# Kernel tuning notes

Hardware: AMD Instinct MI355X
Metric: run time of the kernel (lower is better)

The kernel has to match this reference:

```python
import jax, jax.numpy as jnp
import numpy as np

DIM = 1024
DEPTH = 6
HEADS = 16
MLP = 4096
HEAD_DIM = DIM // HEADS
SCALE = HEAD_DIM ** -0.5
EPS = 1e-5


def _ln(x, g, b):
    m = jnp.mean(x, axis=-1, keepdims=True)
    v = jnp.mean(jnp.square(x - m), axis=-1, keepdims=True)
    return (x - m) * jax.lax.rsqrt(v + EPS) * g + b


def setup_inputs() -> dict:
    key = jax.random.key(0)
    ks = jax.random.split(key, 16)
    B, N = 4, 1024
    s_d = 1.0 / np.sqrt(DIM)
    s_m = 1.0 / np.sqrt(MLP)
    inp = {
        "x1": jax.random.normal(ks[0], (B, N, DIM), jnp.float32),
        "x2": jax.random.normal(ks[1], (B, N, DIM), jnp.float32),
        # stacked per-layer params; Linear weights stored as [in, out]
        "ln1_g": jnp.ones((DEPTH, DIM), jnp.float32),
        "ln1_b": jnp.zeros((DEPTH, DIM), jnp.float32),
        "wq": jax.random.normal(ks[2], (DEPTH, DIM, DIM), jnp.float32) * s_d,
        "wk": jax.random.normal(ks[3], (DEPTH, DIM, DIM), jnp.float32) * s_d,
        "wv": jax.random.normal(ks[4], (DEPTH, DIM, DIM), jnp.float32) * s_d,
        "wo": jax.random.normal(ks[5], (DEPTH, DIM, DIM), jnp.float32) * s_d,
        "bo": jnp.zeros((DEPTH, DIM), jnp.float32),
        "ln2_g": jnp.ones((DEPTH, DIM), jnp.float32),
        "ln2_b": jnp.zeros((DEPTH, DIM), jnp.float32),
        "w1": jax.random.normal(ks[6], (DEPTH, DIM, MLP), jnp.float32) * s_d,
        "b1": jnp.zeros((DEPTH, MLP), jnp.float32),
        "w2": jax.random.normal(ks[7], (DEPTH, MLP, DIM), jnp.float32) * s_m,
        "b2": jnp.zeros((DEPTH, DIM), jnp.float32),
    }
    return inp


def _split_heads(t):
    b, n, _ = t.shape
    return t.reshape(b, n, HEADS, HEAD_DIM).transpose(0, 2, 1, 3)  # b h n d


def reference(x1, x2, ln1_g, ln1_b, wq, wk, wv, wo, bo, ln2_g, ln2_b, w1, b1, w2, b2):
    # dropout disabled (eval mode)
    for i in range(DEPTH):
        # PreNorm(MCA): same LayerNorm params applied to x1 and x2
        n1 = _ln(x1, ln1_g[i], ln1_b[i])
        n2 = _ln(x2, ln1_g[i], ln1_b[i])
        q = _split_heads(n1 @ wq[i])
        k = _split_heads(n2 @ wk[i])
        v = _split_heads(n2 @ wv[i])
        dots = jnp.einsum('bhqd,bhkd->bhqk', q, k) * SCALE
        attn = jax.nn.softmax(dots, axis=-1)
        out = jnp.einsum('bhqk,bhkd->bhqd', attn, v)
        b, h, n, d = out.shape
        out = out.transpose(0, 2, 1, 3).reshape(b, n, h * d)
        x1 = out @ wo[i] + bo[i] + x1
        # PreNorm(FeedForward)
        nf = _ln(x1, ln2_g[i], ln2_b[i])
        hdn = jax.nn.gelu(nf @ w1[i] + b1[i], approximate=False)
        x1 = hdn @ w2[i] + b2[i] + x1
    return x1
```

## Files before the change

kernel.cpp:

```cpp
#include <hip/hip_runtime.h>
#include <stdint.h>

#define N_SEQ 1024
#define N_TOK 4096
#define ATT_SCALE 0.125f

typedef unsigned short u16;
typedef __attribute__((ext_vector_type(8))) short short8;
typedef __attribute__((ext_vector_type(4))) short short4v;
typedef __attribute__((ext_vector_type(4))) float f32x4;

__device__ __forceinline__ u16 f2bf(float f) {
  uint32_t u = __float_as_uint(f);
  u += 0x7fffu + ((u >> 16) & 1u);
  return (u16)(u >> 16);
}

__device__ __forceinline__ void gload16(const void* g, void* lds) {
  __builtin_amdgcn_global_load_lds(
      (const __attribute__((address_space(1))) unsigned int*)g,
      (__attribute__((address_space(3))) unsigned int*)lds, 16, 0, 0);
}

__global__ void copy_f32_kernel(const float* __restrict__ in, float* __restrict__ out) {
  int i = blockIdx.x * 256 + threadIdx.x;
  ((float4*)out)[i] = ((const float4*)in)[i];
}

__global__ __launch_bounds__(256) void tconv_kernel(const float* __restrict__ src,
                                                    u16* __restrict__ dst,
                                                    int K, int NN, size_t dstLS) {
  __shared__ u16 tile[64][68];
  int n0 = blockIdx.x * 64, k0 = blockIdx.y * 64, L = blockIdx.z;
  const float* s = src + (size_t)L * K * NN;
  u16* d = dst + (size_t)L * dstLS;
  int t = threadIdx.x;
  int rr = t >> 4, cc = (t & 15) * 4;
#pragma unroll
  for (int ii = 0; ii < 4; ii++) {
    int kl = rr + ii * 16;
    float4 v = *(const float4*)&s[(size_t)(k0 + kl) * NN + n0 + cc];
    tile[cc + 0][kl] = f2bf(v.x);
    tile[cc + 1][kl] = f2bf(v.y);
    tile[cc + 2][kl] = f2bf(v.z);
    tile[cc + 3][kl] = f2bf(v.w);
  }
  __syncthreads();
#pragma unroll
  for (int ii = 0; ii < 4; ii++) {
    int nl = rr + ii * 16;
    short4v o;
    o.x = (short)tile[nl][cc + 0];
    o.y = (short)tile[nl][cc + 1];
    o.z = (short)tile[nl][cc + 2];
    o.w = (short)tile[nl][cc + 3];
    *(short4v*)&d[(size_t)(n0 + nl) * K + k0 + cc] = o;
  }
}

__global__ __launch_bounds__(256) void ln_kernel(const float* __restrict__ x,
                                                 const float* __restrict__ g,
                                                 const float* __restrict__ b,
                                                 u16* __restrict__ out) {
  int row = blockIdx.x;
  const float* xr = x + (size_t)row * 1024;
  int t = threadIdx.x;
  float4 v = *(const float4*)&xr[t * 4];
  float s = v.x + v.y + v.z + v.w;
  float sq = v.x * v.x + v.y * v.y + v.z * v.z + v.w * v.w;
#pragma unroll
  for (int m = 1; m < 64; m <<= 1) {
    s += __shfl_xor(s, m, 64);
    sq += __shfl_xor(sq, m, 64);
  }
  __shared__ float ps[8];
  int w = t >> 6;
  if ((t & 63) == 0) { ps[w] = s; ps[4 + w] = sq; }
  __syncthreads();
  s = ps[0] + ps[1] + ps[2] + ps[3];
  sq = ps[4] + ps[5] + ps[6] + ps[7];
  float mean = s * (1.0f / 1024.0f);
  float var = sq * (1.0f / 1024.0f) - mean * mean;
  float rs = rsqrtf(var + 1e-5f);
  float4 gv = *(const float4*)&g[t * 4];
  float4 bv = *(const float4*)&b[t * 4];
  short4v o;
  o.x = (short)f2bf((v.x - mean) * rs * gv.x + bv.x);
  o.y = (short)f2bf((v.y - mean) * rs * gv.y + bv.y);
  o.z = (short)f2bf((v.z - mean) * rs * gv.z + bv.z);
  o.w = (short)f2bf((v.w - mean) * rs * gv.w + bv.w);
  *(short4v*)&out[(size_t)row * 1024 + t * 4] = o;
}

template <int BM, int BN, int WM, int WN, int MODE>
__global__ __launch_bounds__(WM * WN * 64, 2) void gemm8(const u16* __restrict__ A,
                                                         const u16* __restrict__ Bt,
                                                         u16* __restrict__ outb,
                                                         float* __restrict__ outf,
                                                         const float* __restrict__ bias,
                                                         const float* __restrict__ resid,
                                                         int N, int K) {
  constexpr int BK = 64;
  constexpr int NW = WM * WN;
  constexpr int T = NW * 64;
  constexpr int WTM = BM / WM, WTN = BN / WN;
  constexpr int FM = WTM / 16, FN = WTN / 16, HM = FM / 2;
  constexpr int AT = BM * BK, BTL = BN * BK;
  constexpr int LA = AT / 8 / T, LB = BTL / 8 / T;
  constexpr int LTOT = LA + LB;
  __shared__ u16 smem[2 * (AT + BTL)];

  int t = threadIdx.x, lane = t & 63, w = t >> 6;
  int wm = w / WN, wn = w % WN;
  const u16* Ag = A + (size_t)(blockIdx.y * BM) * K;
  const u16* Bg = Bt + (size_t)(blockIdx.x * BN) * K;
  f32x4 acc[FM][FN] = {};

  auto stage = [&](int d, int k0) {
    u16* ab = smem + d * (AT + BTL);
    u16* bb = ab + AT;
#pragma unroll
    for (int l = 0; l < LA; l++) {
      int c = (l * NW + w) * 64 + lane;
      int r = c >> 3, s = c & 7;
      gload16(Ag + (size_t)r * K + k0 + ((s ^ (r & 7)) << 3), ab + (l * NW + w) * 512);
    }
#pragma unroll
    for (int l = 0; l < LB; l++) {
      int c = (l * NW + w) * 64 + lane;
      int r = c >> 3, s = c & 7;
      gload16(Bg + (size_t)r * K + k0 + ((s ^ (r & 7)) << 3), bb + (l * NW + w) * 512);
    }
  };

  auto rdA = [&](const u16* ab, int mi, int ks) {
    int rr = wm * WTM + mi * 16 + (lane & 15);
    int j = ks * 4 + (lane >> 4);
    return *(const short8*)&ab[rr * BK + ((j ^ (rr & 7)) << 3)];
  };
  auto rdB = [&](const u16* bb, int ni, int ks) {
    int rr = wn * WTN + ni * 16 + (lane & 15);
    int j = ks * 4 + (lane >> 4);
    return *(const short8*)&bb[rr * BK + ((j ^ (rr & 7)) << 3)];
  };

  const int NT = K / BK;
  stage(0, 0);
  stage(1, BK);
  __builtin_amdgcn_sched_barrier(0);

  int buf = 0;
  for (int tt = 0; tt < NT; tt++) {
    asm volatile("s_waitcnt vmcnt(%0)" ::"n"(LTOT) : "memory");
    __builtin_amdgcn_s_barrier();
    __builtin_amdgcn_sched_barrier(0);
    const u16* ab = smem + buf * (AT + BTL);
    const u16* bb = ab + AT;
    short8 b0[FN], a0lo[HM], a0hi[HM], b1[FN], a1lo[HM], a1hi[HM];
#pragma unroll
    for (int n = 0; n < FN; n++) b0[n] = rdB(bb, n, 0);
#pragma unroll
    for (int m = 0; m < HM; m++) a0lo[m] = rdA(ab, m, 0);
#pragma unroll
    for (int m = 0; m < HM; m++) a0hi[m] = rdA(ab, HM + m, 0);
    asm volatile("s_waitcnt lgkmcnt(%0)" ::"n"(HM) : "memory");
    __builtin_amdgcn_sched_barrier(0);
#pragma unroll
    for (int n = 0; n < FN; n++) b1[n] = rdB(bb, n, 1);
#pragma unroll
    for (int m = 0; m < HM; m++) a1lo[m] = rdA(ab, m, 1);
    __builtin_amdgcn_s_setprio(1);
#pragma unroll
    for (int m = 0; m < HM; m++)
#pragma unroll
      for (int n = 0; n < FN; n++)
        acc[m][n] = __builtin_amdgcn_mfma_f32_16x16x32_bf16(a0lo[m], b0[n], acc[m][n], 0, 0, 0);
    __builtin_amdgcn_s_setprio(0);
    asm volatile("s_waitcnt lgkmcnt(%0)" ::"n"(FN + HM) : "memory");
    __builtin_amdgcn_sched_barrier(0);
#pragma unroll
    for (int m = 0; m < HM; m++) a1hi[m] = rdA(ab, HM + m, 1);
    __builtin_amdgcn_s_setprio(1);
#pragma unroll
    for (int m = 0; m < HM; m++)
#pragma unroll
      for (int n = 0; n < FN; n++)
        acc[HM + m][n] = __builtin_amdgcn_mfma_f32_16x16x32_bf16(a0hi[m], b0[n], acc[HM + m][n], 0, 0, 0);
    __builtin_amdgcn_s_setprio(0);
    asm volatile("s_waitcnt lgkmcnt(%0)" ::"n"(HM) : "memory");
    __builtin_amdgcn_sched_barrier(0);
    __builtin_amdgcn_s_setprio(1);
#pragma unroll
    for (int m = 0; m < HM; m++)
#pragma unroll
      for (int n = 0; n < FN; n++)
        acc[m][n] = __builtin_amdgcn_mfma_f32_16x16x32_bf16(a1lo[m], b1[n], acc[m][n], 0, 0, 0);
    __builtin_amdgcn_s_setprio(0);
    asm volatile("s_waitcnt lgkmcnt(0)" ::: "memory");
    __builtin_amdgcn_sched_barrier(0);
    __builtin_amdgcn_s_barrier();
    __builtin_amdgcn_sched_barrier(0);
    stage(buf, ((tt + 2) % NT) * BK);
    __builtin_amdgcn_sched_barrier(0);
    __builtin_amdgcn_s_setprio(1);
#pragma unroll
    for (int m = 0; m < HM; m++)
#pragma unroll
      for (int n = 0; n < FN; n++)
        acc[HM + m][n] = __builtin_amdgcn_mfma_f32_16x16x32_bf16(a1hi[m], b1[n], acc[HM + m][n], 0, 0, 0);
    __builtin_amdgcn_s_setprio(0);
    buf ^= 1;
  }

  int r0 = blockIdx.y * BM + wm * WTM + ((lane >> 4) << 2);
  int c0 = blockIdx.x * BN + wn * WTN + (lane & 15);
#pragma unroll
  for (int mi = 0; mi < FM; mi++) {
#pragma unroll
    for (int r = 0; r < 4; r++) {
      size_t row = (size_t)(r0 + mi * 16 + r);
#pragma unroll
      for (int ni = 0; ni < FN; ni++) {
        size_t col = (size_t)(c0 + ni * 16);
        size_t idx = row * N + col;
        float val = acc[mi][ni][r];
        if (MODE == 0) {
          outb[idx] = f2bf(val);
        } else if (MODE == 1) {
          outf[idx] = val + bias[col] + resid[idx];
        } else {
          float xg = val + bias[col];
          outb[idx] = f2bf(0.5f * xg * (1.0f + erff(xg * 0.70710678f)));
        }
      }
    }
  }
}

__global__ __launch_bounds__(256, 4) void attn_kernel(const u16* __restrict__ qb,
                                                      const u16* __restrict__ kvb,
                                                      u16* __restrict__ ob) {
  int qt = blockIdx.x, bh = blockIdx.y;
  int b = bh >> 4, h = bh & 15;
  int t = threadIdx.x, lane = t & 63, w = t >> 6;
  __shared__ u16 Qs[64 * 64];
  __shared__ u16 Ks[64 * 64];
  __shared__ u16 Vt[64 * 64];
  __shared__ u16 Ps[4][16 * 64];

  const u16* qbase = qb + (size_t)b * N_SEQ * 1024 + h * 64;
  const u16* kbase = kvb + (size_t)b * N_SEQ * 2048 + h * 64;
  const u16* vbase = kbase + 1024;
  u16* obase = ob + (size_t)b * N_SEQ * 1024 + h * 64;

  int r = t >> 2, c = (t & 3) * 16;
  {
    const u16* src = qbase + (size_t)(qt * 64 + r) * 1024 + c;
    *(short8*)&Qs[r * 64 + c] = *(const short8*)src;
    *(short8*)&Qs[r * 64 + c + 8] = *(const short8*)(src + 8);
  }
  short8 kreg0, kreg1, vreg0, vreg1;
  {
    const u16* ksrc = kbase + (size_t)r * 2048 + c;
    kreg0 = *(const short8*)ksrc;
    kreg1 = *(const short8*)(ksrc + 8);
    const u16* vsrc = vbase + (size_t)r * 2048 + c;
    vreg0 = *(const short8*)vsrc;
    vreg1 = *(const short8*)(vsrc + 8);
  }
  __syncthreads();
  short8 qa0 = *(const short8*)&Qs[(w * 16 + (lane & 15)) * 64 + (lane >> 4) * 8];
  short8 qa1 = *(const short8*)&Qs[(w * 16 + (lane & 15)) * 64 + 32 + (lane >> 4) * 8];

  f32x4 o[4] = {};
  float m_r[4] = {-1e30f, -1e30f, -1e30f, -1e30f};
  float l_r[4] = {0.0f, 0.0f, 0.0f, 0.0f};

  for (int kt = 0; kt < 16; kt++) {
    if (kt > 0) __syncthreads();
    {
      int jj0 = c >> 3;
      *(short8*)&Ks[r * 64 + ((jj0 ^ (r & 7)) << 3)] = kreg0;
      *(short8*)&Ks[r * 64 + (((jj0 + 1) ^ (r & 7)) << 3)] = kreg1;
#pragma unroll
      for (int j = 0; j < 8; j++) {
        int row = c + j, rowb = c + 8 + j;
        Vt[row * 64 + (((r >> 3) ^ (row & 7)) << 3) + (r & 7)] = (u16)vreg0[j];
        Vt[rowb * 64 + (((r >> 3) ^ (rowb & 7)) << 3) + (r & 7)] = (u16)vreg1[j];
      }
    }
    __syncthreads();
    if (kt < 15) {
      const u16* ksrc = kbase + (size_t)((kt + 1) * 64 + r) * 2048 + c;
      kreg0 = *(const short8*)ksrc;
      kreg1 = *(const short8*)(ksrc + 8);
      const u16* vsrc = vbase + (size_t)((kt + 1) * 64 + r) * 2048 + c;
      vreg0 = *(const short8*)vsrc;
      vreg1 = *(const short8*)(vsrc + 8);
    }

    f32x4 s[4] = {};
#pragma unroll
    for (int kb = 0; kb < 4; kb++) {
      int key = kb * 16 + (lane & 15);
      int jj = lane >> 4;
      short8 k0 = *(const short8*)&Ks[key * 64 + ((jj ^ (key & 7)) << 3)];
      short8 k1 = *(const short8*)&Ks[key * 64 + (((4 + jj) ^ (key & 7)) << 3)];
      s[kb] = __builtin_amdgcn_mfma_f32_16x16x32_bf16(qa0, k0, s[kb], 0, 0, 0);
      s[kb] = __builtin_amdgcn_mfma_f32_16x16x32_bf16(qa1, k1, s[kb], 0, 0, 0);
    }
    float fac[4], rowsum[4];
#pragma unroll
    for (int rr = 0; rr < 4; rr++) {
      float a = fmaxf(fmaxf(s[0][rr], s[1][rr]), fmaxf(s[2][rr], s[3][rr])) * ATT_SCALE;
      a = fmaxf(a, __shfl_xor(a, 1, 64));
      a = fmaxf(a, __shfl_xor(a, 2, 64));
      a = fmaxf(a, __shfl_xor(a, 4, 64));
      a = fmaxf(a, __shfl_xor(a, 8, 64));
      float mn = fmaxf(m_r[rr], a);
      fac[rr] = __expf(m_r[rr] - mn);
      m_r[rr] = mn;
      rowsum[rr] = 0.0f;
    }
#pragma unroll
    for (int kb = 0; kb < 4; kb++) {
      int chunk = 2 * kb + ((lane & 15) >> 3);
#pragma unroll
      for (int rr = 0; rr < 4; rr++) {
        float p = __expf(s[kb][rr] * ATT_SCALE - m_r[rr]);
        rowsum[rr] += p;
        int row = (lane >> 4) * 4 + rr;
        Ps[w][row * 64 + ((chunk ^ (row & 7)) << 3) + (lane & 7)] = f2bf(p);
      }
    }
#pragma unroll
    for (int rr = 0; rr < 4; rr++) {
      float rs = rowsum[rr];
      rs += __shfl_xor(rs, 1, 64);
      rs += __shfl_xor(rs, 2, 64);
      rs += __shfl_xor(rs, 4, 64);
      rs += __shfl_xor(rs, 8, 64);
      l_r[rr] = l_r[rr] * fac[rr] + rs;
      o[0][rr] *= fac[rr];
      o[1][rr] *= fac[rr];
      o[2][rr] *= fac[rr];
      o[3][rr] *= fac[rr];
    }
#pragma unroll
    for (int ks = 0; ks < 2; ks++) {
      int rowp = lane & 15;
      int jj = 4 * ks + (lane >> 4);
      short8 pf = *(const short8*)&Ps[w][rowp * 64 + ((jj ^ (rowp & 7)) << 3)];
#pragma unroll
      for (int db = 0; db < 4; db++) {
        int row = db * 16 + (lane & 15);
        short8 vf = *(const short8*)&Vt[row * 64 + ((jj ^ (row & 7)) << 3)];
        o[db] = __builtin_amdgcn_mfma_f32_16x16x32_bf16(pf, vf, o[db], 0, 0, 0);
      }
    }
  }
#pragma unroll
  for (int rr = 0; rr < 4; rr++) {
    float inv = 1.0f / l_r[rr];
    size_t row = (size_t)(qt * 64 + w * 16 + (lane >> 4) * 4 + rr);
#pragma unroll
    for (int db = 0; db < 4; db++)
      obase[row * 1024 + db * 16 + (lane & 15)] = f2bf(o[db][rr] * inv);
  }
}

extern "C" void kernel_launch(void* const* d_in, const int* in_sizes, int n_in,
                              void* d_out, int out_size, void* d_ws, size_t ws_size,
                              hipStream_t stream) {
  const float* x1 = (const float*)d_in[0];
  const float* x2 = (const float*)d_in[1];
  const float* ln1_g = (const float*)d_in[2];
  const float* ln1_b = (const float*)d_in[3];
  const float* wq = (const float*)d_in[4];
  const float* wk = (const float*)d_in[5];
  const float* wv = (const float*)d_in[6];
  const float* wo = (const float*)d_in[7];
  const float* bo = (const float*)d_in[8];
  const float* ln2_g = (const float*)d_in[9];
  const float* ln2_b = (const float*)d_in[10];
  const float* w1 = (const float*)d_in[11];
  const float* b1 = (const float*)d_in[12];
  const float* w2 = (const float*)d_in[13];
  const float* b2 = (const float*)d_in[14];
  float* xout = (float*)d_out;

  u16* p = (u16*)d_ws;
  u16* wqt = p;  p += (size_t)6 * 1024 * 1024;
  u16* kvt = p;  p += (size_t)6 * 2048 * 1024;
  u16* wot = p;  p += (size_t)6 * 1024 * 1024;
  u16* w1t = p;  p += (size_t)6 * 4096 * 1024;
  u16* w2t = p;  p += (size_t)6 * 1024 * 4096;
  u16* n1 = p;   p += (size_t)N_TOK * 1024;
  u16* n2 = p;   p += (size_t)N_TOK * 1024;
  u16* qbuf = p; p += (size_t)N_TOK * 1024;
  u16* kvbuf = p; p += (size_t)N_TOK * 2048;
  u16* ao = p;   p += (size_t)N_TOK * 1024;
  u16* hid = p;  p += (size_t)N_TOK * 4096;

  dim3 blk(256);
  tconv_kernel<<<dim3(16, 16, 6), blk, 0, stream>>>(wq, wqt, 1024, 1024, (size_t)1024 * 1024);
  tconv_kernel<<<dim3(16, 16, 6), blk, 0, stream>>>(wk, kvt, 1024, 1024, (size_t)2048 * 1024);
  tconv_kernel<<<dim3(16, 16, 6), blk, 0, stream>>>(wv, kvt + (size_t)1024 * 1024, 1024, 1024, (size_t)2048 * 1024);
  tconv_kernel<<<dim3(16, 16, 6), blk, 0, stream>>>(wo, wot, 1024, 1024, (size_t)1024 * 1024);
  tconv_kernel<<<dim3(64, 16, 6), blk, 0, stream>>>(w1, w1t, 1024, 4096, (size_t)4096 * 1024);
  tconv_kernel<<<dim3(16, 64, 6), blk, 0, stream>>>(w2, w2t, 4096, 1024, (size_t)1024 * 4096);
  copy_f32_kernel<<<4096, blk, 0, stream>>>(x1, xout);

  for (int i = 0; i < 6; i++) {
    ln_kernel<<<N_TOK, blk, 0, stream>>>(xout, ln1_g + i * 1024, ln1_b + i * 1024, n1);
    ln_kernel<<<N_TOK, blk, 0, stream>>>(x2, ln1_g + i * 1024, ln1_b + i * 1024, n2);
    gemm8<128, 64, 2, 2, 0><<<dim3(16, 32), dim3(256), 0, stream>>>(
        n1, wqt + (size_t)i * 1024 * 1024, qbuf, nullptr, nullptr, nullptr, 1024, 1024);
    gemm8<128, 128, 2, 2, 0><<<dim3(16, 32), dim3(256), 0, stream>>>(
        n2, kvt + (size_t)i * 2048 * 1024, kvbuf, nullptr, nullptr, nullptr, 2048, 1024);
    attn_kernel<<<dim3(16, 64), blk, 0, stream>>>(qbuf, kvbuf, ao);
    gemm8<128, 64, 2, 2, 1><<<dim3(16, 32), dim3(256), 0, stream>>>(
        ao, wot + (size_t)i * 1024 * 1024, nullptr, xout, bo + i * 1024, xout, 1024, 1024);
    ln_kernel<<<N_TOK, blk, 0, stream>>>(xout, ln2_g + i * 1024, ln2_b + i * 1024, n1);
    gemm8<128, 128, 2, 2, 2><<<dim3(32, 32), dim3(256), 0, stream>>>(
        n1, w1t + (size_t)i * 4096 * 1024, hid, nullptr, b1 + i * 4096, nullptr, 4096, 1024);
    gemm8<128, 64, 2, 2, 1><<<dim3(16, 32), dim3(256), 0, stream>>>(
        hid, w2t + (size_t)i * 1024 * 4096, nullptr, xout, b2 + i * 1024, xout, 1024, 4096);
  }
}
```

Before: 1.581 ms.

## Replace hand-scheduled GEMM main loop with simple double-buffered loop and per-shape occupancy

Drops the hand-interleaved GEMM main loop, which used explicit waitcnt, sched_barrier, setprio and a two-tile-ahead prefetch. In its place is a plain double-buffered loop: prefetch the next tile, load all fragments, issue the MFMAs, then __syncthreads. Launch bounds are now a template parameter, allowing 3 blocks per CU for the 128x64 tiles. The aim is simpler code the compiler can schedule, plus higher occupancy on the narrower GEMMs. In exchange, the hand-tuned overlap of LDS reads with MFMAs is lost.

```diff
diff --git a/kernel.cpp b/kernel.cpp
--- a/kernel.cpp
+++ b/kernel.cpp
@@ -92,22 +92,21 @@
   *(short4v*)&out[(size_t)row * 1024 + t * 4] = o;
 }
 
-template <int BM, int BN, int WM, int WN, int MODE>
-__global__ __launch_bounds__(WM * WN * 64, 2) void gemm8(const u16* __restrict__ A,
-                                                         const u16* __restrict__ Bt,
-                                                         u16* __restrict__ outb,
-                                                         float* __restrict__ outf,
-                                                         const float* __restrict__ bias,
-                                                         const float* __restrict__ resid,
-                                                         int N, int K) {
+template <int BM, int BN, int WM, int WN, int MAXB, int MODE>
+__global__ __launch_bounds__(WM * WN * 64, MAXB) void gemmS(const u16* __restrict__ A,
+                                                            const u16* __restrict__ Bt,
+                                                            u16* __restrict__ outb,
+                                                            float* __restrict__ outf,
+                                                            const float* __restrict__ bias,
+                                                            const float* __restrict__ resid,
+                                                            int N, int K) {
   constexpr int BK = 64;
   constexpr int NW = WM * WN;
   constexpr int T = NW * 64;
   constexpr int WTM = BM / WM, WTN = BN / WN;
-  constexpr int FM = WTM / 16, FN = WTN / 16, HM = FM / 2;
+  constexpr int FM = WTM / 16, FN = WTN / 16;
   constexpr int AT = BM * BK, BTL = BN * BK;
   constexpr int LA = AT / 8 / T, LB = BTL / 8 / T;
-  constexpr int LTOT = LA + LB;
   __shared__ u16 smem[2 * (AT + BTL)];
 
   int t = threadIdx.x, lane = t & 63, w = t >> 6;
@@ -146,69 +145,30 @@
 
   const int NT = K / BK;
   stage(0, 0);
-  stage(1, BK);
-  __builtin_amdgcn_sched_barrier(0);
+  __syncthreads();
 
   int buf = 0;
   for (int tt = 0; tt < NT; tt++) {
-    asm volatile("s_waitcnt vmcnt(%0)" ::"n"(LTOT) : "memory");
-    __builtin_amdgcn_s_barrier();
-    __builtin_amdgcn_sched_barrier(0);
+    if (tt + 1 < NT) stage(buf ^ 1, (tt + 1) * BK);
     const u16* ab = smem + buf * (AT + BTL);
     const u16* bb = ab + AT;
-    short8 b0[FN], a0lo[HM], a0hi[HM], b1[FN], a1lo[HM], a1hi[HM];
-#pragma unroll
-    for (int n = 0; n < FN; n++) b0[n] = rdB(bb, n, 0);
-#pragma unroll
-    for (int m = 0; m < HM; m++) a0lo[m] = rdA(ab, m, 0);
-#pragma unroll
-    for (int m = 0; m < HM; m++) a0hi[m] = rdA(ab, HM + m, 0);
-    asm volatile("s_waitcnt lgkmcnt(%0)" ::"n"(HM) : "memory");
-    __builtin_amdgcn_sched_barrier(0);
-#pragma unroll
-    for (int n = 0; n < FN; n++) b1[n] = rdB(bb, n, 1);
-#pragma unroll
-    for (int m = 0; m < HM; m++) a1lo[m] = rdA(ab, m, 1);
-    __builtin_amdgcn_s_setprio(1);
-#pragma unroll
-    for (int m = 0; m < HM; m++)
-#pragma unroll
-      for (int n = 0; n < FN; n++)
-        acc[m][n] = __builtin_amdgcn_mfma_f32_16x16x32_bf16(a0lo[m], b0[n], acc[m][n], 0, 0, 0);
-    __builtin_amdgcn_s_setprio(0);
-    asm volatile("s_waitcnt lgkmcnt(%0)" ::"n"(FN + HM) : "memory");
-    __builtin_amdgcn_sched_barrier(0);
-#pragma unroll
-    for (int m = 0; m < HM; m++) a1hi[m] = rdA(ab, HM + m, 1);
-    __builtin_amdgcn_s_setprio(1);
-#pragma unroll
-    for (int m = 0; m < HM; m++)
-#pragma unroll
-      for (int n = 0; n < FN; n++)
-        acc[HM + m][n] = __builtin_amdgcn_mfma_f32_16x16x32_bf16(a0hi[m], b0[n], acc[HM + m][n], 0, 0, 0);
-    __builtin_amdgcn_s_setprio(0);
-    asm volatile("s_waitcnt lgkmcnt(%0)" ::"n"(HM) : "memory");
-    __builtin_amdgcn_sched_barrier(0);
-    __builtin_amdgcn_s_setprio(1);
-#pragma unroll
-    for (int m = 0; m < HM; m++)
-#pragma unroll
-      for (int n = 0; n < FN; n++)
-        acc[m][n] = __builtin_amdgcn_mfma_f32_16x16x32_bf16(a1lo[m], b1[n], acc[m][n], 0, 0, 0);
-    __builtin_amdgcn_s_setprio(0);
-    asm volatile("s_waitcnt lgkmcnt(0)" ::: "memory");
-    __builtin_amdgcn_sched_barrier(0);
-    __builtin_amdgcn_s_barrier();
-    __builtin_amdgcn_sched_barrier(0);
-    stage(buf, ((tt + 2) % NT) * BK);
-    __builtin_amdgcn_sched_barrier(0);
-    __builtin_amdgcn_s_setprio(1);
-#pragma unroll
-    for (int m = 0; m < HM; m++)
-#pragma unroll
-      for (int n = 0; n < FN; n++)
-        acc[HM + m][n] = __builtin_amdgcn_mfma_f32_16x16x32_bf16(a1hi[m], b1[n], acc[HM + m][n], 0, 0, 0);
-    __builtin_amdgcn_s_setprio(0);
+    short8 af[2][FM], bfr[2][FN];
+#pragma unroll
+    for (int ks = 0; ks < 2; ks++) {
+#pragma unroll
+      for (int mi = 0; mi < FM; mi++) af[ks][mi] = rdA(ab, mi, ks);
+#pragma unroll
+      for (int ni = 0; ni < FN; ni++) bfr[ks][ni] = rdB(bb, ni, ks);
+    }
+#pragma unroll
+    for (int ks = 0; ks < 2; ks++)
+#pragma unroll
+      for (int mi = 0; mi < FM; mi++)
+#pragma unroll
+        for (int ni = 0; ni < FN; ni++)
+          acc[mi][ni] = __builtin_amdgcn_mfma_f32_16x16x32_bf16(af[ks][mi], bfr[ks][ni],
+                                                                acc[mi][ni], 0, 0, 0);
+    __syncthreads();
     buf ^= 1;
   }
 
@@ -414,17 +374,17 @@
   for (int i = 0; i < 6; i++) {
     ln_kernel<<<N_TOK, blk, 0, stream>>>(xout, ln1_g + i * 1024, ln1_b + i * 1024, n1);
     ln_kernel<<<N_TOK, blk, 0, stream>>>(x2, ln1_g + i * 1024, ln1_b + i * 1024, n2);
-    gemm8<128, 64, 2, 2, 0><<<dim3(16, 32), dim3(256), 0, stream>>>(
+    gemmS<128, 64, 2, 2, 3, 0><<<dim3(16, 32), dim3(256), 0, stream>>>(
         n1, wqt + (size_t)i * 1024 * 1024, qbuf, nullptr, nullptr, nullptr, 1024, 1024);
-    gemm8<128, 128, 2, 2, 0><<<dim3(16, 32), dim3(256), 0, stream>>>(
+    gemmS<128, 128, 2, 2, 2, 0><<<dim3(16, 32), dim3(256), 0, stream>>>(
         n2, kvt + (size_t)i * 2048 * 1024, kvbuf, nullptr, nullptr, nullptr, 2048, 1024);
     attn_kernel<<<dim3(16, 64), blk, 0, stream>>>(qbuf, kvbuf, ao);
-    gemm8<128, 64, 2, 2, 1><<<dim3(16, 32), dim3(256), 0, stream>>>(
+    gemmS<128, 64, 2, 2, 3, 1><<<dim3(16, 32), dim3(256), 0, stream>>>(
         ao, wot + (size_t)i * 1024 * 1024, nullptr, xout, bo + i * 1024, xout, 1024, 1024);
     ln_kernel<<<N_TOK, blk, 0, stream>>>(xout, ln2_g + i * 1024, ln2_b + i * 1024, n1);
-    gemm8<128, 128, 2, 2, 2><<<dim3(32, 32), dim3(256), 0, stream>>>(
+    gemmS<128, 128, 2, 2, 2, 2><<<dim3(32, 32), dim3(256), 0, stream>>>(
         n1, w1t + (size_t)i * 4096 * 1024, hid, nullptr, b1 + i * 4096, nullptr, 4096, 1024);
-    gemm8<128, 64, 2, 2, 1><<<dim3(16, 32), dim3(256), 0, stream>>>(
+    gemmS<128, 64, 2, 2, 3, 1><<<dim3(16, 32), dim3(256), 0, stream>>>(
         hid, w2t + (size_t)i * 1024 * 4096, nullptr, xout, b2 + i * 1024, xout, 1024, 4096);
   }
 }
```

After: 1.709 ms. +8.1%, slower.

## Switch GEMM to triple-buffered BK=32 pipeline with three waves per SIMD

Applied to the files above, without the earlier changes.

The GEMM kernel drops from two LDS buffers of BK=64 to three buffers of BK=32 and prefetches three tiles ahead. The swizzle and fragment reads are rewritten for the 4-chunk row layout, and launch bounds now target three blocks per CU. The KV projection also moves to a 64x128 tile with twice as many blocks. The aim is deeper latency hiding and higher occupancy, at the cost of more barriers per unit of K and half as much MFMA work between each sync.

```diff
diff --git a/kernel.cpp b/kernel.cpp
--- a/kernel.cpp
+++ b/kernel.cpp
@@ -93,14 +93,14 @@
 }
 
 template <int BM, int BN, int WM, int WN, int MODE>
-__global__ __launch_bounds__(WM * WN * 64, 2) void gemm8(const u16* __restrict__ A,
+__global__ __launch_bounds__(WM * WN * 64, 3) void gemm3(const u16* __restrict__ A,
                                                          const u16* __restrict__ Bt,
                                                          u16* __restrict__ outb,
                                                          float* __restrict__ outf,
                                                          const float* __restrict__ bias,
                                                          const float* __restrict__ resid,
                                                          int N, int K) {
-  constexpr int BK = 64;
+  constexpr int BK = 32;
   constexpr int NW = WM * WN;
   constexpr int T = NW * 64;
   constexpr int WTM = BM / WM, WTN = BN / WN;
@@ -108,7 +108,8 @@
   constexpr int AT = BM * BK, BTL = BN * BK;
   constexpr int LA = AT / 8 / T, LB = BTL / 8 / T;
   constexpr int LTOT = LA + LB;
-  __shared__ u16 smem[2 * (AT + BTL)];
+  constexpr int SLOT = AT + BTL;
+  __shared__ u16 smem[3 * SLOT];
 
   int t = threadIdx.x, lane = t & 63, w = t >> 6;
   int wm = w / WN, wn = w % WN;
@@ -117,76 +118,51 @@
   f32x4 acc[FM][FN] = {};
 
   auto stage = [&](int d, int k0) {
-    u16* ab = smem + d * (AT + BTL);
+    u16* ab = smem + d * SLOT;
     u16* bb = ab + AT;
 #pragma unroll
     for (int l = 0; l < LA; l++) {
       int c = (l * NW + w) * 64 + lane;
-      int r = c >> 3, s = c & 7;
-      gload16(Ag + (size_t)r * K + k0 + ((s ^ (r & 7)) << 3), ab + (l * NW + w) * 512);
+      int r = c >> 2, s = c & 3;
+      gload16(Ag + (size_t)r * K + k0 + ((s ^ (r & 3)) << 3), ab + (l * NW + w) * 512);
     }
 #pragma unroll
     for (int l = 0; l < LB; l++) {
       int c = (l * NW + w) * 64 + lane;
-      int r = c >> 3, s = c & 7;
-      gload16(Bg + (size_t)r * K + k0 + ((s ^ (r & 7)) << 3), bb + (l * NW + w) * 512);
+      int r = c >> 2, s = c & 3;
+      gload16(Bg + (size_t)r * K + k0 + ((s ^ (r & 3)) << 3), bb + (l * NW + w) * 512);
     }
   };
 
-  auto rdA = [&](const u16* ab, int mi, int ks) {
+  auto rdA = [&](const u16* ab, int mi) {
     int rr = wm * WTM + mi * 16 + (lane & 15);
-    int j = ks * 4 + (lane >> 4);
-    return *(const short8*)&ab[rr * BK + ((j ^ (rr & 7)) << 3)];
+    int j = lane >> 4;
+    return *(const short8*)&ab[rr * BK + ((j ^ (rr & 3)) << 3)];
   };
-  auto rdB = [&](const u16* bb, int ni, int ks) {
+  auto rdB = [&](const u16* bb, int ni) {
     int rr = wn * WTN + ni * 16 + (lane & 15);
-    int j = ks * 4 + (lane >> 4);
-    return *(const short8*)&bb[rr * BK + ((j ^ (rr & 7)) << 3)];
+    int j = lane >> 4;
+    return *(const short8*)&bb[rr * BK + ((j ^ (rr & 3)) << 3)];
   };
 
   const int NT = K / BK;
   stage(0, 0);
   stage(1, BK);
+  stage(2, 2 * BK);
   __builtin_amdgcn_sched_barrier(0);
 
-  int buf = 0;
+  int sl = 0;
   for (int tt = 0; tt < NT; tt++) {
-    asm volatile("s_waitcnt vmcnt(%0)" ::"n"(LTOT) : "memory");
+    asm volatile("s_waitcnt vmcnt(%0)" ::"n"(2 * LTOT) : "memory");
     __builtin_amdgcn_s_barrier();
     __builtin_amdgcn_sched_barrier(0);
-    const u16* ab = smem + buf * (AT + BTL);
+    const u16* ab = smem + sl * SLOT;
     const u16* bb = ab + AT;
-    short8 b0[FN], a0lo[HM], a0hi[HM], b1[FN], a1lo[HM], a1hi[HM];
-#pragma unroll
-    for (int n = 0; n < FN; n++) b0[n] = rdB(bb, n, 0);
-#pragma unroll
-    for (int m = 0; m < HM; m++) a0lo[m] = rdA(ab, m, 0);
-#pragma unroll
-    for (int m = 0; m < HM; m++) a0hi[m] = rdA(ab, HM + m, 0);
-    asm volatile("s_waitcnt lgkmcnt(%0)" ::"n"(HM) : "memory");
-    __builtin_amdgcn_sched_barrier(0);
-#pragma unroll
-    for (int n = 0; n < FN; n++) b1[n] = rdB(bb, n, 1);
-#pragma unroll
-    for (int m = 0; m < HM; m++) a1lo[m] = rdA(ab, m, 1);
-    __builtin_amdgcn_s_setprio(1);
-#pragma unroll
-    for (int m = 0; m < HM; m++)
-#pragma unroll
-      for (int n = 0; n < FN; n++)
-        acc[m][n] = __builtin_amdgcn_mfma_f32_16x16x32_bf16(a0lo[m], b0[n], acc[m][n], 0, 0, 0);
-    __builtin_amdgcn_s_setprio(0);
-    asm volatile("s_waitcnt lgkmcnt(%0)" ::"n"(FN + HM) : "memory");
-    __builtin_amdgcn_sched_barrier(0);
-#pragma unroll
-    for (int m = 0; m < HM; m++) a1hi[m] = rdA(ab, HM + m, 1);
-    __builtin_amdgcn_s_setprio(1);
-#pragma unroll
-    for (int m = 0; m < HM; m++)
-#pragma unroll
-      for (int n = 0; n < FN; n++)
-        acc[HM + m][n] = __builtin_amdgcn_mfma_f32_16x16x32_bf16(a0hi[m], b0[n], acc[HM + m][n], 0, 0, 0);
-    __builtin_amdgcn_s_setprio(0);
+    short8 bf[FN], am[FM];
+#pragma unroll
+    for (int n = 0; n < FN; n++) bf[n] = rdB(bb, n);
+#pragma unroll
+    for (int m = 0; m < FM; m++) am[m] = rdA(ab, m);
     asm volatile("s_waitcnt lgkmcnt(%0)" ::"n"(HM) : "memory");
     __builtin_amdgcn_sched_barrier(0);
     __builtin_amdgcn_s_setprio(1);
@@ -194,23 +170,24 @@
     for (int m = 0; m < HM; m++)
 #pragma unroll
       for (int n = 0; n < FN; n++)
-        acc[m][n] = __builtin_amdgcn_mfma_f32_16x16x32_bf16(a1lo[m], b1[n], acc[m][n], 0, 0, 0);
+        acc[m][n] = __builtin_amdgcn_mfma_f32_16x16x32_bf16(am[m], bf[n], acc[m][n], 0, 0, 0);
     __builtin_amdgcn_s_setprio(0);
     asm volatile("s_waitcnt lgkmcnt(0)" ::: "memory");
     __builtin_amdgcn_sched_barrier(0);
     __builtin_amdgcn_s_barrier();
     __builtin_amdgcn_sched_barrier(0);
-    stage(buf, ((tt + 2) % NT) * BK);
+    stage(sl, ((tt + 3) % NT) * BK);
     __builtin_amdgcn_sched_barrier(0);
     __builtin_amdgcn_s_setprio(1);
 #pragma unroll
-    for (int m = 0; m < HM; m++)
+    for (int m = HM; m < FM; m++)
 #pragma unroll
       for (int n = 0; n < FN; n++)
-        acc[HM + m][n] = __builtin_amdgcn_mfma_f32_16x16x32_bf16(a1hi[m], b1[n], acc[HM + m][n], 0, 0, 0);
+        acc[m][n] = __builtin_amdgcn_mfma_f32_16x16x32_bf16(am[m], bf[n], acc[m][n], 0, 0, 0);
     __builtin_amdgcn_s_setprio(0);
-    buf ^= 1;
-  }
+    sl = (sl + 1 == 3) ? 0 : sl + 1;
+  }
+  asm volatile("s_waitcnt vmcnt(0)" ::: "memory");
 
   int r0 = blockIdx.y * BM + wm * WTM + ((lane >> 4) << 2);
   int c0 = blockIdx.x * BN + wn * WTN + (lane & 15);
@@ -414,17 +391,17 @@
   for (int i = 0; i < 6; i++) {
     ln_kernel<<<N_TOK, blk, 0, stream>>>(xout, ln1_g + i * 1024, ln1_b + i * 1024, n1);
     ln_kernel<<<N_TOK, blk, 0, stream>>>(x2, ln1_g + i * 1024, ln1_b + i * 1024, n2);
-    gemm8<128, 64, 2, 2, 0><<<dim3(16, 32), dim3(256), 0, stream>>>(
+    gemm3<128, 64, 2, 2, 0><<<dim3(16, 32), blk, 0, stream>>>(
         n1, wqt + (size_t)i * 1024 * 1024, qbuf, nullptr, nullptr, nullptr, 1024, 1024);
-    gemm8<128, 128, 2, 2, 0><<<dim3(16, 32), dim3(256), 0, stream>>>(
+    gemm3<64, 128, 2, 2, 0><<<dim3(16, 64), blk, 0, stream>>>(
         n2, kvt + (size_t)i * 2048 * 1024, kvbuf, nullptr, nullptr, nullptr, 2048, 1024);
     attn_kernel<<<dim3(16, 64), blk, 0, stream>>>(qbuf, kvbuf, ao);
-    gemm8<128, 64, 2, 2, 1><<<dim3(16, 32), dim3(256), 0, stream>>>(
+    gemm3<128, 64, 2, 2, 1><<<dim3(16, 32), blk, 0, stream>>>(
         ao, wot + (size_t)i * 1024 * 1024, nullptr, xout, bo + i * 1024, xout, 1024, 1024);
     ln_kernel<<<N_TOK, blk, 0, stream>>>(xout, ln2_g + i * 1024, ln2_b + i * 1024, n1);
-    gemm8<128, 128, 2, 2, 2><<<dim3(32, 32), dim3(256), 0, stream>>>(
+    gemm3<128, 128, 2, 2, 2><<<dim3(32, 32), blk, 0, stream>>>(
         n1, w1t + (size_t)i * 4096 * 1024, hid, nullptr, b1 + i * 4096, nullptr, 4096, 1024);
-    gemm8<128, 64, 2, 2, 1><<<dim3(16, 32), dim3(256), 0, stream>>>(
+    gemm3<128, 64, 2, 2, 1><<<dim3(16, 32), blk, 0, stream>>>(
         hid, w2t + (size_t)i * 1024 * 4096, nullptr, xout, b2 + i * 1024, xout, 1024, 4096);
   }
 }
```

Result: slower. 1.805 ms (+14.2%).

## Add BK=32 double-buffered gemm kernel for the MLP up-projection

Applied to the files above, without the earlier changes.

Introduces a new 128x128 GEMM kernel with a 32-wide K step, double-buffered LDS staging via global_load_lds, and launch bounds targeting three blocks per CU. The W1+GELU GEMM is switched to it. The aim is more occupancy and overlap of loads with MFMA work. In exchange it drops whatever LDS swizzling and epilogue vectorisation gemm8 had, risking LDS bank conflicts and scalar, uncoalesced stores. The other launch edits only swap dim3(256) for the identical blk.

```diff
diff --git a/kernel.cpp b/kernel.cpp
--- a/kernel.cpp
+++ b/kernel.cpp
@@ -90,6 +90,88 @@
   o.z = (short)f2bf((v.z - mean) * rs * gv.z + bv.z);
   o.w = (short)f2bf((v.w - mean) * rs * gv.w + bv.w);
   *(short4v*)&out[(size_t)row * 1024 + t * 4] = o;
+}
+
+template <int MODE>
+__global__ __launch_bounds__(256, 3) void gemmM(const u16* __restrict__ A,
+                                                const u16* __restrict__ Bt,
+                                                u16* __restrict__ outb,
+                                                float* __restrict__ outf,
+                                                const float* __restrict__ bias,
+                                                const float* __restrict__ resid,
+                                                int N, int K) {
+  constexpr int AT = 128 * 32;
+  __shared__ u16 smem[2 * 2 * AT];
+
+  int t = threadIdx.x, lane = t & 63, w = t >> 6;
+  int wm = w >> 1, wn = w & 1;
+  const u16* Ag = A + (size_t)(blockIdx.y * 128) * K;
+  const u16* Bg = Bt + (size_t)(blockIdx.x * 128) * K;
+  f32x4 acc[4][4] = {};
+
+  auto stage = [&](int d, int k0) {
+    u16* ab = smem + d * 2 * AT;
+    u16* bb = ab + AT;
+#pragma unroll
+    for (int l = 0; l < 2; l++) {
+      int c = l * 256 + t;
+      gload16(Ag + (size_t)(c >> 2) * K + k0 + (c & 3) * 8, ab + c * 8);
+    }
+#pragma unroll
+    for (int l = 0; l < 2; l++) {
+      int c = l * 256 + t;
+      gload16(Bg + (size_t)(c >> 2) * K + k0 + (c & 3) * 8, bb + c * 8);
+    }
+  };
+
+  const int NT = K / 32;
+  stage(0, 0);
+  __syncthreads();
+
+  int buf = 0;
+  for (int tt = 0; tt < NT; tt++) {
+    if (tt + 1 < NT) stage(buf ^ 1, (tt + 1) * 32);
+    const u16* ab = smem + buf * 2 * AT;
+    const u16* bb = ab + AT;
+    short8 af[4], bf[4];
+#pragma unroll
+    for (int mi = 0; mi < 4; mi++)
+      af[mi] = *(const short8*)&ab[(wm * 64 + mi * 16 + (lane & 15)) * 32 + (lane >> 4) * 8];
+#pragma unroll
+    for (int ni = 0; ni < 4; ni++)
+      bf[ni] = *(const short8*)&bb[(wn * 64 + ni * 16 + (lane & 15)) * 32 + (lane >> 4) * 8];
+#pragma unroll
+    for (int mi = 0; mi < 4; mi++)
+#pragma unroll
+      for (int ni = 0; ni < 4; ni++)
+        acc[mi][ni] = __builtin_amdgcn_mfma_f32_16x16x32_bf16(af[mi], bf[ni], acc[mi][ni], 0, 0, 0);
+    __syncthreads();
+    buf ^= 1;
+  }
+
+  int r0 = blockIdx.y * 128 + wm * 64 + ((lane >> 4) << 2);
+  int c0 = blockIdx.x * 128 + wn * 64 + (lane & 15);
+#pragma unroll
+  for (int mi = 0; mi < 4; mi++) {
+#pragma unroll
+    for (int r = 0; r < 4; r++) {
+      size_t row = (size_t)(r0 + mi * 16 + r);
+#pragma unroll
+      for (int ni = 0; ni < 4; ni++) {
+        size_t col = (size_t)(c0 + ni * 16);
+        size_t idx = row * N + col;
+        float val = acc[mi][ni][r];
+        if (MODE == 0) {
+          outb[idx] = f2bf(val);
+        } else if (MODE == 1) {
+          outf[idx] = val + bias[col] + resid[idx];
+        } else {
+          float xg = val + bias[col];
+          outb[idx] = f2bf(0.5f * xg * (1.0f + erff(xg * 0.70710678f)));
+        }
+      }
+    }
+  }
 }
 
 template <int BM, int BN, int WM, int WN, int MODE>
@@ -414,17 +496,17 @@
   for (int i = 0; i < 6; i++) {
     ln_kernel<<<N_TOK, blk, 0, stream>>>(xout, ln1_g + i * 1024, ln1_b + i * 1024, n1);
     ln_kernel<<<N_TOK, blk, 0, stream>>>(x2, ln1_g + i * 1024, ln1_b + i * 1024, n2);
-    gemm8<128, 64, 2, 2, 0><<<dim3(16, 32), dim3(256), 0, stream>>>(
+    gemm8<128, 64, 2, 2, 0><<<dim3(16, 32), blk, 0, stream>>>(
         n1, wqt + (size_t)i * 1024 * 1024, qbuf, nullptr, nullptr, nullptr, 1024, 1024);
-    gemm8<128, 128, 2, 2, 0><<<dim3(16, 32), dim3(256), 0, stream>>>(
+    gemm8<128, 128, 2, 2, 0><<<dim3(16, 32), blk, 0, stream>>>(
         n2, kvt + (size_t)i * 2048 * 1024, kvbuf, nullptr, nullptr, nullptr, 2048, 1024);
     attn_kernel<<<dim3(16, 64), blk, 0, stream>>>(qbuf, kvbuf, ao);
-    gemm8<128, 64, 2, 2, 1><<<dim3(16, 32), dim3(256), 0, stream>>>(
+    gemm8<128, 64, 2, 2, 1><<<dim3(16, 32), blk, 0, stream>>>(
         ao, wot + (size_t)i * 1024 * 1024, nullptr, xout, bo + i * 1024, xout, 1024, 1024);
     ln_kernel<<<N_TOK, blk, 0, stream>>>(xout, ln2_g + i * 1024, ln2_b + i * 1024, n1);
-    gemm8<128, 128, 2, 2, 2><<<dim3(32, 32), dim3(256), 0, stream>>>(
+    gemmM<2><<<dim3(32, 32), blk, 0, stream>>>(
         n1, w1t + (size_t)i * 4096 * 1024, hid, nullptr, b1 + i * 4096, nullptr, 4096, 1024);
-    gemm8<128, 64, 2, 2, 1><<<dim3(16, 32), dim3(256), 0, stream>>>(
+    gemm8<128, 64, 2, 2, 1><<<dim3(16, 32), blk, 0, stream>>>(
         hid, w2t + (size_t)i * 1024 * 4096, nullptr, xout, b2 + i * 1024, xout, 1024, 4096);
   }
 }
```

Result: no change. 1.575 ms (-0.4%).
